# Kernel tuning notes

Measured on AMD Instinct MI355X. Metric: run time of the kernel, lower is better.

## Reference

```python
import jax, jax.numpy as jnp
import numpy as np


def log_g(x):
    # log of g(x) where g(x) = x + 0.5 for x >= 0 else sigmoid(x)
    return jnp.where(x >= 0, jnp.log(jnp.where(x >= 0, x, 0.0) + 0.5), -jax.nn.softplus(-x))


def mingru_layer(x, h0, W, b):
    # x: (B,S,Din), h0: (B,1,H) positive, W: (2H,Din), b: (2H,)
    gh = jnp.einsum('bsd,ed->bse', x, W) + b
    gate, hidden = jnp.split(gh, 2, axis=-1)
    log_z = -jax.nn.softplus(-gate)        # log sigmoid(gate)
    log_coeffs = -jax.nn.softplus(gate)    # log (1 - sigmoid(gate))
    log_values = jnp.concatenate([jnp.log(h0), log_z + log_g(hidden)], axis=1)  # (B,S+1,H)
    a_star = jnp.pad(jnp.cumsum(log_coeffs, axis=1), ((0, 0), (1, 0), (0, 0)))  # (B,S+1,H)
    log_h = a_star + jax.lax.cumlogsumexp(log_values - a_star, axis=1)
    return jnp.exp(log_h)[:, 1:]  # (B,S,H)


def setup_inputs() -> dict:
    key = jax.random.key(0)
    ks = jax.random.split(key, 6)
    B, S, D, H = 8, 2048, 1024, 1024
    L = 2
    s = 0.02
    return {
        'x': jax.random.normal(ks[0], (B, S, D), jnp.float32),
        'h': jax.random.uniform(ks[1], (L, B, 1, H), jnp.float32, 0.05, 1.0),
        'w0': jax.random.normal(ks[2], (2 * H, D), jnp.float32) * s,
        'b0': jax.random.normal(ks[3], (2 * H,), jnp.float32) * s,
        'w1': jax.random.normal(ks[4], (2 * H, H), jnp.float32) * s,
        'b1': jax.random.normal(ks[5], (2 * H,), jnp.float32) * s,
    }


def reference(x, h, w0, b0, w1, b1):
    # layer 0 (residual, align = Identity since input_dims == hidden_dims)
    out0 = mingru_layer(x, h[0], w0, b0)
    h0_final = out0[:, -1:]
    inp = out0 + x
    # layer 1 (last layer: residual, no dropout after)
    out1 = mingru_layer(inp, h[1], w1, b1)
    h1_final = out1[:, -1:]
    out = out1 + inp
    h_final = jnp.stack([h0_final, h1_final])  # (L,B,1,H)
    return out, h_final
```

## Files before the change

kernel.cpp:

```cpp
#include <hip/hip_runtime.h>
#include <hip/hip_bf16.h>
#include <cstdint>
#include <cstddef>

#define GAS __attribute__((address_space(1)))
#define LAS __attribute__((address_space(3)))

typedef __attribute__((ext_vector_type(8))) __bf16 bf16x8;
typedef __attribute__((ext_vector_type(4))) float f32x4;

constexpr int kB = 8, kS = 2048, kK = 1024, kH = 1024;
constexpr int kM = kB * kS;
constexpr int kN2 = 2 * kH;
constexpr int kChunks = 64;
constexpr int kSc = kS / kChunks;

constexpr int BM = 256, BN = 256, BK = 32;
constexpr int NKT = kK / BK;

constexpr size_t kOffXb   = 0;
constexpr size_t kOffW0   = 33554432;
constexpr size_t kOffW1   = 37748736;
constexpr size_t kOffA    = 41943040;
constexpr size_t kOffG    = 75497472;
constexpr size_t kOffCA   = 109051904;
constexpr size_t kOffCV   = 111149056;
constexpr size_t kOffHst  = 113246208;
constexpr size_t kWsNeed  = 115343360;

__device__ __forceinline__ ushort f2bf(float f) {
    union { float f; uint32_t u; } v; v.f = f;
    uint32_t r = v.u + 0x7FFFu + ((v.u >> 16) & 1u);
    return (ushort)(r >> 16);
}
__device__ __forceinline__ float bf2f(ushort u) {
    union { uint32_t u; float f; } v; v.u = (uint32_t)u << 16;
    return v.f;
}

__global__ void cvt_bf16_kernel(const float* __restrict__ src, ushort* __restrict__ dst, int n4) {
    int i = blockIdx.x * blockDim.x + threadIdx.x;
    if (i >= n4) return;
    f32x4 v = *reinterpret_cast<const f32x4*>(src + (size_t)i * 4);
    ushort4 o;
    o.x = f2bf(v.x); o.y = f2bf(v.y); o.z = f2bf(v.z); o.w = f2bf(v.w);
    *reinterpret_cast<ushort4*>(dst + (size_t)i * 4) = o;
}

__global__ __launch_bounds__(512, 1)
void gemm_epi_kernel(const ushort* __restrict__ A, const ushort* __restrict__ W,
                     const float* __restrict__ bias,
                     ushort* __restrict__ abuf, ushort* __restrict__ gbuf)
{
    __shared__ ushort smem[65536];

    const int tid  = threadIdx.x;
    const int lane = tid & 63;
    const int wv   = tid >> 6;
    const int wm   = wv >> 2;
    const int wn   = wv & 3;

    const int bid = blockIdx.x;
    const int sid = (bid & 7) * 64 + (bid >> 3);
    const int tm  = sid >> 3;
    const int tn  = sid & 7;
    const int m0  = tm * BM;
    const int n0  = tn * BN;

    f32x4 acc[8][4];
#pragma unroll
    for (int i = 0; i < 8; ++i)
#pragma unroll
        for (int j = 0; j < 4; ++j) acc[i][j] = (f32x4){0.f, 0.f, 0.f, 0.f};

    const int srow = wv * 16 + (lane >> 2);
    const int scol = (lane & 3) * 8;

    const ushort* ga0 = A + (size_t)(m0 + srow) * kK + scol;
    const ushort* ga1 = ga0 + (size_t)128 * kK;
    const ushort* gb0 = W + (size_t)(n0 + srow) * kK + scol;
    const ushort* gb1 = gb0 + (size_t)128 * kK;

    char* lds = (char*)smem;
    const int ldsw = wv * 1024;

    const int rb   = (lane & 15) * 64 + (lane >> 4) * 16;
    const int aoff = wm * 8192 + rb;
    const int boff = 16384 + wn * 4096 + rb;

#define STAGE(BUF) do {                                                          \
    __builtin_amdgcn_global_load_lds((const GAS void*)(ga0),                     \
        (LAS void*)(lds + (BUF) * 32768 + ldsw),          16, 0, 0);             \
    __builtin_amdgcn_global_load_lds((const GAS void*)(ga1),                     \
        (LAS void*)(lds + (BUF) * 32768 + 8192  + ldsw),  16, 0, 0);             \
    __builtin_amdgcn_global_load_lds((const GAS void*)(gb0),                     \
        (LAS void*)(lds + (BUF) * 32768 + 16384 + ldsw),  16, 0, 0);             \
    __builtin_amdgcn_global_load_lds((const GAS void*)(gb1),                     \
        (LAS void*)(lds + (BUF) * 32768 + 24576 + ldsw),  16, 0, 0);             \
    ga0 += BK; ga1 += BK; gb0 += BK; gb1 += BK;                                  \
  } while (0)

#define COMPUTE(BUF) do {                                                        \
    const char* lb_ = lds + (BUF) * 32768;                                       \
    bf16x8 bf_[4], af_[8];                                                       \
    _Pragma("unroll")                                                            \
    for (int nf_ = 0; nf_ < 4; ++nf_)                                            \
        bf_[nf_] = *reinterpret_cast<const bf16x8*>(lb_ + boff + nf_ * 1024);    \
    _Pragma("unroll")                                                            \
    for (int mf_ = 0; mf_ < 8; ++mf_)                                            \
        af_[mf_] = *reinterpret_cast<const bf16x8*>(lb_ + aoff + mf_ * 1024);    \
    __builtin_amdgcn_s_setprio(1);                                               \
    _Pragma("unroll")                                                            \
    for (int mf_ = 0; mf_ < 8; ++mf_)                                            \
        _Pragma("unroll")                                                        \
        for (int nf_ = 0; nf_ < 4; ++nf_)                                        \
            acc[mf_][nf_] = __builtin_amdgcn_mfma_f32_16x16x32_bf16(             \
                af_[mf_], bf_[nf_], acc[mf_][nf_], 0, 0, 0);                     \
    __builtin_amdgcn_s_setprio(0);                                               \
  } while (0)

#define TILE(BUF, STBUF) do {                                                    \
    asm volatile("s_waitcnt vmcnt(4)" ::: "memory");                             \
    __builtin_amdgcn_s_barrier();                                                \
    __builtin_amdgcn_sched_barrier(0);                                           \
    STAGE(STBUF);                                                                \
    COMPUTE(BUF);                                                                \
  } while (0)

    STAGE(0);
    STAGE(1);

    for (int g = 0; g < 7; ++g) {
        TILE(0, 2);
        TILE(1, 3);
        TILE(2, 0);
        TILE(3, 1);
    }
    TILE(0, 2);
    TILE(1, 3);
    asm volatile("s_waitcnt vmcnt(4)" ::: "memory");
    __builtin_amdgcn_s_barrier();
    __builtin_amdgcn_sched_barrier(0);
    COMPUTE(2);
    asm volatile("s_waitcnt vmcnt(0)" ::: "memory");
    __builtin_amdgcn_s_barrier();
    __builtin_amdgcn_sched_barrier(0);
    COMPUTE(3);

#undef STAGE
#undef COMPUTE
#undef TILE

    const bool isGate = (tn < 4);
    ushort* outp = isGate ? abuf : gbuf;
    const int ncol0 = (isGate ? tn : tn - 4) * 256 + wn * 64;
    float bn[4];
#pragma unroll
    for (int nf = 0; nf < 4; ++nf) bn[nf] = bias[n0 + wn * 64 + nf * 16 + (lane & 15)];
#pragma unroll
    for (int mf = 0; mf < 8; ++mf) {
#pragma unroll
        for (int i = 0; i < 4; ++i) {
            const int m = m0 + wm * 128 + mf * 16 + (lane >> 4) * 4 + i;
            ushort* rowp = outp + (size_t)m * kH + ncol0;
#pragma unroll
            for (int nf = 0; nf < 4; ++nf) {
                float val = acc[mf][nf][i] + bn[nf];
                float r;
                if (isGate) r = 1.f / (1.f + __expf(val));
                else        r = (val >= 0.f) ? val + 0.5f : 1.f / (1.f + __expf(-val));
                rowp[nf * 16 + (lane & 15)] = f2bf(r);
            }
        }
    }
}

__global__ void scan_reduce_kernel(const ushort* __restrict__ abuf, const ushort* __restrict__ gbuf,
                                   float* __restrict__ cA, float* __restrict__ cV)
{
    int idx = blockIdx.x * 256 + threadIdx.x;
    int chg = idx & 255;
    int c   = (idx >> 8) & (kChunks - 1);
    int b   = idx >> 14;
    size_t ch = (size_t)chg * 4;
    size_t row = (size_t)b * kS + (size_t)c * kSc;
    const ushort* ap = abuf + row * kH + ch;
    const ushort* gp = gbuf + row * kH + ch;
    f32x4 A = (f32x4){1.f, 1.f, 1.f, 1.f};
    f32x4 V = (f32x4){0.f, 0.f, 0.f, 0.f};
    for (int t = 0; t < kSc; ++t) {
        ushort4 au = *reinterpret_cast<const ushort4*>(ap);
        ushort4 gu = *reinterpret_cast<const ushort4*>(gp);
        f32x4 a = (f32x4){bf2f(au.x), bf2f(au.y), bf2f(au.z), bf2f(au.w)};
        f32x4 g = (f32x4){bf2f(gu.x), bf2f(gu.y), bf2f(gu.z), bf2f(gu.w)};
        V = a * V + (1.f - a) * g;
        A = A * a;
        ap += kH; gp += kH;
    }
    size_t o = ((size_t)(b * kChunks + c) * kH) + ch;
    *reinterpret_cast<f32x4*>(cA + o) = A;
    *reinterpret_cast<f32x4*>(cV + o) = V;
}

__global__ void scan_chunks_kernel(const float* __restrict__ cA, const float* __restrict__ cV,
                                   const float* __restrict__ h0, float* __restrict__ hstart,
                                   float* __restrict__ hfin)
{
    int idx = blockIdx.x * 256 + threadIdx.x;
    int chg = idx & 255;
    int b   = idx >> 8;
    size_t ch = (size_t)chg * 4;
    f32x4 h = *reinterpret_cast<const f32x4*>(h0 + (size_t)b * kH + ch);
    for (int c = 0; c < kChunks; ++c) {
        size_t o = ((size_t)(b * kChunks + c) * kH) + ch;
        *reinterpret_cast<f32x4*>(hstart + o) = h;
        f32x4 A = *reinterpret_cast<const f32x4*>(cA + o);
        f32x4 V = *reinterpret_cast<const f32x4*>(cV + o);
        h = A * h + V;
    }
    *reinterpret_cast<f32x4*>(hfin + (size_t)b * kH + ch) = h;
}

template<bool WRITE_F32>
__global__ void scan_apply_kernel(const ushort* __restrict__ abuf, const ushort* __restrict__ gbuf,
                                  const float* __restrict__ hstart, const ushort* __restrict__ addin,
                                  void* __restrict__ outp)
{
    int idx = blockIdx.x * 256 + threadIdx.x;
    int chg = idx & 255;
    int c   = (idx >> 8) & (kChunks - 1);
    int b   = idx >> 14;
    size_t ch = (size_t)chg * 4;
    size_t row = (size_t)b * kS + (size_t)c * kSc;
    size_t base = row * kH + ch;
    f32x4 h = *reinterpret_cast<const f32x4*>(hstart + ((size_t)(b * kChunks + c) * kH) + ch);
    const ushort* ap = abuf + base;
    const ushort* gp = gbuf + base;
    for (int t = 0; t < kSc; ++t) {
        ushort4 au = *reinterpret_cast<const ushort4*>(ap);
        ushort4 gu = *reinterpret_cast<const ushort4*>(gp);
        f32x4 a = (f32x4){bf2f(au.x), bf2f(au.y), bf2f(au.z), bf2f(au.w)};
        f32x4 g = (f32x4){bf2f(gu.x), bf2f(gu.y), bf2f(gu.z), bf2f(gu.w)};
        h = a * h + (1.f - a) * g;
        ushort4 xu = *reinterpret_cast<const ushort4*>(addin + base + (size_t)t * kH);
        f32x4 r = (f32x4){bf2f(xu.x), bf2f(xu.y), bf2f(xu.z), bf2f(xu.w)};
        f32x4 o = h + r;
        if (WRITE_F32) {
            *reinterpret_cast<f32x4*>((float*)outp + base + (size_t)t * kH) = o;
        } else {
            ushort4 ob;
            ob.x = f2bf(o.x); ob.y = f2bf(o.y); ob.z = f2bf(o.z); ob.w = f2bf(o.w);
            *reinterpret_cast<ushort4*>((ushort*)outp + base + (size_t)t * kH) = ob;
        }
        ap += kH; gp += kH;
    }
}

extern "C" void kernel_launch(void* const* d_in, const int* in_sizes, int n_in,
                              void* d_out, int out_size, void* d_ws, size_t ws_size,
                              hipStream_t stream)
{
    const float* x  = (const float*)d_in[0];
    const float* h  = (const float*)d_in[1];
    const float* w0 = (const float*)d_in[2];
    const float* b0 = (const float*)d_in[3];
    const float* w1 = (const float*)d_in[4];
    const float* b1 = (const float*)d_in[5];
    float* out = (float*)d_out;
    char* ws = (char*)d_ws;

    if (ws_size < kWsNeed) return;

    ushort* xb   = (ushort*)(ws + kOffXb);
    ushort* inpb = (ushort*)(ws + kOffXb);
    ushort* w0b  = (ushort*)(ws + kOffW0);
    ushort* w1b  = (ushort*)(ws + kOffW1);
    ushort* abuf = (ushort*)(ws + kOffA);
    ushort* gbuf = (ushort*)(ws + kOffG);
    float*  cA   = (float*)(ws + kOffCA);
    float*  cV   = (float*)(ws + kOffCV);
    float*  hst  = (float*)(ws + kOffHst);

    float* out_h = out + (size_t)kM * kH;

    cvt_bf16_kernel<<<(kM * kK / 4 + 255) / 256, 256, 0, stream>>>(x, xb, kM * kK / 4);
    cvt_bf16_kernel<<<(kN2 * kK / 4 + 255) / 256, 256, 0, stream>>>(w0, w0b, kN2 * kK / 4);
    cvt_bf16_kernel<<<(kN2 * kK / 4 + 255) / 256, 256, 0, stream>>>(w1, w1b, kN2 * kK / 4);

    const int gemm_grid = (kM / BM) * (kN2 / BN);

    gemm_epi_kernel<<<gemm_grid, 512, 0, stream>>>(xb, w0b, b0, abuf, gbuf);
    scan_reduce_kernel<<<512, 256, 0, stream>>>(abuf, gbuf, cA, cV);
    scan_chunks_kernel<<<8, 256, 0, stream>>>(cA, cV, h, hst, out_h);
    scan_apply_kernel<false><<<512, 256, 0, stream>>>(abuf, gbuf, hst, xb, inpb);

    gemm_epi_kernel<<<gemm_grid, 512, 0, stream>>>(inpb, w1b, b1, abuf, gbuf);
    scan_reduce_kernel<<<512, 256, 0, stream>>>(abuf, gbuf, cA, cV);
    scan_chunks_kernel<<<8, 256, 0, stream>>>(cA, cV, h + (size_t)kB * kH, hst, out_h + (size_t)kB * kH);
    scan_apply_kernel<true><<<512, 256, 0, stream>>>(abuf, gbuf, hst, inpb, out);
}
```

Before: 290.1 us.

## Swizzle LDS GEMM tiles and split each K-step into two barrier-synced phases

Applies an XOR swizzle to the 16-byte slot used both when global loads write into LDS and when fragments are read back, to cut LDS bank conflicts. Each K tile is now processed in two halves of the M fragments, with the global-to-LDS stage split into A and B parts interleaved between the halves. Explicit barriers and lgkmcnt waits are added so the phases run in lockstep across waves. This adds more barriers per tile and lowers fragment register pressure, with risk that the extra synchronisation offsets the overlap gain.

```diff
diff --git a/kernel.cpp b/kernel.cpp
--- a/kernel.cpp
+++ b/kernel.cpp
@@ -73,8 +73,9 @@
 #pragma unroll
         for (int j = 0; j < 4; ++j) acc[i][j] = (f32x4){0.f, 0.f, 0.f, 0.f};
 
-    const int srow = wv * 16 + (lane >> 2);
-    const int scol = (lane & 3) * 8;
+    const int srow  = wv * 16 + (lane >> 2);
+    const int sslot = (lane & 3) ^ ((lane >> 3) & 3);
+    const int scol  = sslot * 8;
 
     const ushort* ga0 = A + (size_t)(m0 + srow) * kK + scol;
     const ushort* ga1 = ga0 + (size_t)128 * kK;
@@ -84,51 +85,79 @@
     char* lds = (char*)smem;
     const int ldsw = wv * 1024;
 
-    const int rb   = (lane & 15) * 64 + (lane >> 4) * 16;
-    const int aoff = wm * 8192 + rb;
-    const int boff = 16384 + wn * 4096 + rb;
-
-#define STAGE(BUF) do {                                                          \
+    const int rslot = (lane >> 4) ^ ((lane >> 1) & 3);
+    const int rb    = (lane & 15) * 64 + rslot * 16;
+    const int aoff  = wm * 8192 + rb;
+    const int boff  = 16384 + wn * 4096 + rb;
+
+#define VMWAIT(N) asm volatile("s_waitcnt vmcnt(" #N ")" ::: "memory")
+
+#define STAGE_A(SBUF) do {                                                       \
     __builtin_amdgcn_global_load_lds((const GAS void*)(ga0),                     \
-        (LAS void*)(lds + (BUF) * 32768 + ldsw),          16, 0, 0);             \
+        (LAS void*)(lds + (SBUF) * 32768 + ldsw),          16, 0, 0);            \
     __builtin_amdgcn_global_load_lds((const GAS void*)(ga1),                     \
-        (LAS void*)(lds + (BUF) * 32768 + 8192  + ldsw),  16, 0, 0);             \
+        (LAS void*)(lds + (SBUF) * 32768 + 8192  + ldsw),  16, 0, 0);            \
+  } while (0)
+
+#define STAGE_B(SBUF) do {                                                       \
     __builtin_amdgcn_global_load_lds((const GAS void*)(gb0),                     \
-        (LAS void*)(lds + (BUF) * 32768 + 16384 + ldsw),  16, 0, 0);             \
+        (LAS void*)(lds + (SBUF) * 32768 + 16384 + ldsw),  16, 0, 0);            \
     __builtin_amdgcn_global_load_lds((const GAS void*)(gb1),                     \
-        (LAS void*)(lds + (BUF) * 32768 + 24576 + ldsw),  16, 0, 0);             \
+        (LAS void*)(lds + (SBUF) * 32768 + 24576 + ldsw),  16, 0, 0);            \
     ga0 += BK; ga1 += BK; gb0 += BK; gb1 += BK;                                  \
   } while (0)
 
-#define COMPUTE(BUF) do {                                                        \
-    const char* lb_ = lds + (BUF) * 32768;                                       \
-    bf16x8 bf_[4], af_[8];                                                       \
+#define TILE_GEN(BUF, SA, SB, EW) do {                                           \
+    bf16x8 bf_[4], af_[4];                                                       \
     _Pragma("unroll")                                                            \
     for (int nf_ = 0; nf_ < 4; ++nf_)                                            \
-        bf_[nf_] = *reinterpret_cast<const bf16x8*>(lb_ + boff + nf_ * 1024);    \
-    _Pragma("unroll")                                                            \
-    for (int mf_ = 0; mf_ < 8; ++mf_)                                            \
-        af_[mf_] = *reinterpret_cast<const bf16x8*>(lb_ + aoff + mf_ * 1024);    \
+        bf_[nf_] = *reinterpret_cast<const bf16x8*>(                             \
+            lds + (BUF) * 32768 + boff + nf_ * 1024);                            \
+    _Pragma("unroll")                                                            \
+    for (int mf_ = 0; mf_ < 4; ++mf_)                                            \
+        af_[mf_] = *reinterpret_cast<const bf16x8*>(                             \
+            lds + (BUF) * 32768 + aoff + mf_ * 1024);                            \
+    SA;                                                                          \
+    __builtin_amdgcn_s_barrier();                                                \
+    asm volatile("s_waitcnt lgkmcnt(0)" ::: "memory");                           \
+    __builtin_amdgcn_sched_barrier(0);                                           \
     __builtin_amdgcn_s_setprio(1);                                               \
     _Pragma("unroll")                                                            \
-    for (int mf_ = 0; mf_ < 8; ++mf_)                                            \
+    for (int mf_ = 0; mf_ < 4; ++mf_)                                            \
         _Pragma("unroll")                                                        \
         for (int nf_ = 0; nf_ < 4; ++nf_)                                        \
             acc[mf_][nf_] = __builtin_amdgcn_mfma_f32_16x16x32_bf16(             \
                 af_[mf_], bf_[nf_], acc[mf_][nf_], 0, 0, 0);                     \
     __builtin_amdgcn_s_setprio(0);                                               \
+    __builtin_amdgcn_s_barrier();                                                \
+    _Pragma("unroll")                                                            \
+    for (int mf_ = 0; mf_ < 4; ++mf_)                                            \
+        af_[mf_] = *reinterpret_cast<const bf16x8*>(                             \
+            lds + (BUF) * 32768 + aoff + 4096 + mf_ * 1024);                     \
+    SB;                                                                          \
+    __builtin_amdgcn_s_barrier();                                                \
+    asm volatile("s_waitcnt lgkmcnt(0)" ::: "memory");                           \
+    __builtin_amdgcn_sched_barrier(0);                                           \
+    __builtin_amdgcn_s_setprio(1);                                               \
+    _Pragma("unroll")                                                            \
+    for (int mf_ = 0; mf_ < 4; ++mf_)                                            \
+        _Pragma("unroll")                                                        \
+        for (int nf_ = 0; nf_ < 4; ++nf_)                                        \
+            acc[4 + mf_][nf_] = __builtin_amdgcn_mfma_f32_16x16x32_bf16(         \
+                af_[mf_], bf_[nf_], acc[4 + mf_][nf_], 0, 0, 0);                 \
+    __builtin_amdgcn_s_setprio(0);                                               \
+    EW;                                                                          \
+    __builtin_amdgcn_s_barrier();                                                \
   } while (0)
 
-#define TILE(BUF, STBUF) do {                                                    \
-    asm volatile("s_waitcnt vmcnt(4)" ::: "memory");                             \
-    __builtin_amdgcn_s_barrier();                                                \
-    __builtin_amdgcn_sched_barrier(0);                                           \
-    STAGE(STBUF);                                                                \
-    COMPUTE(BUF);                                                                \
-  } while (0)
-
-    STAGE(0);
-    STAGE(1);
+#define TILE(BUF, SBUF) TILE_GEN(BUF, STAGE_A(SBUF), STAGE_B(SBUF), VMWAIT(4))
+#define TAIL0(BUF)      TILE_GEN(BUF, (void)0, (void)0, VMWAIT(0))
+#define TAIL1(BUF)      TILE_GEN(BUF, (void)0, (void)0, (void)0)
+
+    STAGE_A(0); STAGE_B(0);
+    STAGE_A(1); STAGE_B(1);
+    VMWAIT(4);
+    __builtin_amdgcn_s_barrier();
 
     for (int g = 0; g < 7; ++g) {
         TILE(0, 2);
@@ -138,18 +167,16 @@
     }
     TILE(0, 2);
     TILE(1, 3);
-    asm volatile("s_waitcnt vmcnt(4)" ::: "memory");
-    __builtin_amdgcn_s_barrier();
-    __builtin_amdgcn_sched_barrier(0);
-    COMPUTE(2);
-    asm volatile("s_waitcnt vmcnt(0)" ::: "memory");
-    __builtin_amdgcn_s_barrier();
-    __builtin_amdgcn_sched_barrier(0);
-    COMPUTE(3);
-
-#undef STAGE
-#undef COMPUTE
+    TAIL0(2);
+    TAIL1(3);
+
 #undef TILE
+#undef TAIL0
+#undef TAIL1
+#undef TILE_GEN
+#undef STAGE_A
+#undef STAGE_B
+#undef VMWAIT
 
     const bool isGate = (tn < 4);
     ushort* outp = isGate ? abuf : gbuf;
```

After: 289.4 us. About the same (-0.2%).
